# Performance work log

Hardware: AMD Instinct MI355X
Metric: run time of the kernel (lower is better)

## Reference

```python
import jax, jax.numpy as jnp
import numpy as np

D_MODEL = 1024
NUM_HEADS = 16
DEPTH = D_MODEL // NUM_HEADS


def setup_inputs() -> dict:
    key = jax.random.key(0)
    k_x, k_wqkv, k_bqkv, k_wp, k_bp = jax.random.split(key, 5)
    B, N = 2, 2048
    x = jax.random.normal(k_x, (B, N, D_MODEL), dtype=jnp.float32)
    scale = 1.0 / np.sqrt(D_MODEL)
    Wqkv = jax.random.normal(k_wqkv, (D_MODEL, 3 * D_MODEL), dtype=jnp.float32) * scale
    bqkv = jnp.zeros((3 * D_MODEL,), dtype=jnp.float32)
    Wproj = jax.random.normal(k_wp, (D_MODEL, D_MODEL), dtype=jnp.float32) * scale
    bproj = jnp.zeros((D_MODEL,), dtype=jnp.float32)
    return {"x": x, "Wqkv": Wqkv, "bqkv": bqkv, "Wproj": Wproj, "bproj": bproj}


def reference(x, Wqkv, bqkv, Wproj, bproj):
    B, N, C = x.shape
    # QKV projection; original layout: [B, N, H, depth, 3] -> transpose to [B, 3, H, N, depth]
    qkv = x @ Wqkv + bqkv                      # [B, N, 3C]
    qkv = qkv.reshape(B, N, NUM_HEADS, DEPTH, 3)
    qkv = jnp.transpose(qkv, (0, 4, 2, 1, 3))  # [B, 3, H, N, depth]
    q, k, v = qkv[:, 0], qkv[:, 1], qkv[:, 2]  # each [B, H, N, depth]
    # scaled dot-product attention (full N x N scores, as in the original)
    scale = 1.0 / jnp.sqrt(jnp.asarray(DEPTH, dtype=x.dtype))
    attn = jnp.einsum("bhnd,bhmd->bhnm", q, k) * scale
    attn = jax.nn.softmax(attn.astype(jnp.float32), axis=-1).astype(x.dtype)
    out = jnp.einsum("bhnm,bhmd->bhnd", attn, v)  # [B, H, N, depth]
    out = jnp.transpose(out, (0, 2, 1, 3)).reshape(B, N, C)
    return out @ Wproj + bproj
```

## Files before the change

kernel.cpp:

```cpp
#include <hip/hip_runtime.h>
#include <stdint.h>

#define D_MODEL 1024
#define NHEADS  16
#define DEPTH   64
#define BATCH   2
#define SEQ     2048
#define M_TOK   (BATCH*SEQ)

typedef __attribute__((ext_vector_type(8)))  short short8;
typedef __attribute__((ext_vector_type(4)))  float f32x4;
typedef __attribute__((ext_vector_type(16))) float f32x16;
typedef __attribute__((ext_vector_type(4)))  unsigned int uint4v;

#if defined(__has_builtin)
#if __has_builtin(__builtin_amdgcn_exp2f)
#define EXP2(x) __builtin_amdgcn_exp2f(x)
#endif
#endif
#ifndef EXP2
#define EXP2(x) exp2f(x)
#endif

__device__ __forceinline__ unsigned short f2bf(float f) {
  unsigned int u = __float_as_uint(f);
  u += 0x7fffu + ((u >> 16) & 1u);
  return (unsigned short)(u >> 16);
}

__device__ __forceinline__ unsigned int cvt_pk_bf16(float lo, float hi) {
  unsigned int r;
  asm("v_cvt_pk_bf16_f32 %0, %1, %2" : "=v"(r) : "v"(lo), "v"(hi));
  return r;
}

__device__ __forceinline__ void gload_lds16(const unsigned short* g, unsigned short* l) {
  __builtin_amdgcn_global_load_lds((const __attribute__((address_space(1))) void*)g,
                                   (__attribute__((address_space(3))) void*)l, 16, 0, 0);
}

__global__ void mha_prep(const float* __restrict__ x, const float* __restrict__ Wqkv,
                         const float* __restrict__ Wproj,
                         unsigned short* __restrict__ xb,
                         unsigned short* __restrict__ wqkT,
                         unsigned short* __restrict__ wvT,
                         unsigned short* __restrict__ wpT) {
  __shared__ float tile[32][33];
  int id = blockIdx.x, t = threadIdx.x;
  if (id < 2048) {
    int i = (id * 256 + t) * 8;
    float4 a = *(const float4*)(x + i);
    float4 b = *(const float4*)(x + i + 4);
    uint4 r;
    r.x = (unsigned)f2bf(a.x) | ((unsigned)f2bf(a.y) << 16);
    r.y = (unsigned)f2bf(a.z) | ((unsigned)f2bf(a.w) << 16);
    r.z = (unsigned)f2bf(b.x) | ((unsigned)f2bf(b.y) << 16);
    r.w = (unsigned)f2bf(b.z) | ((unsigned)f2bf(b.w) << 16);
    *(uint4*)(xb + i) = r;
  } else if (id < 5120) {
    int b = id - 2048;
    int c0 = (b % 96) * 32, k0 = (b / 96) * 32;
    int tx = t & 31, ty = t >> 5;
    for (int i = ty; i < 32; i += 8)
      tile[i][tx] = Wqkv[(size_t)(k0 + i) * 3072 + c0 + tx];
    __syncthreads();
    for (int i = ty; i < 32; i += 8) {
      int c = c0 + i;
      int hd = c / 3;
      int s = c - hd * 3;
      unsigned short v = f2bf(tile[tx][i]);
      if (s < 2) wqkT[(size_t)(s * 1024 + hd) * 1024 + k0 + tx] = v;
      else       wvT [(size_t)hd * 1024 + k0 + tx] = v;
    }
  } else {
    int b = id - 5120;
    int c0 = (b & 31) * 32, k0 = (b >> 5) * 32;
    int tx = t & 31, ty = t >> 5;
    for (int i = ty; i < 32; i += 8)
      tile[i][tx] = Wproj[(size_t)(k0 + i) * 1024 + c0 + tx];
    __syncthreads();
    for (int i = ty; i < 32; i += 8)
      wpT[(size_t)(c0 + i) * 1024 + k0 + tx] = f2bf(tile[tx][i]);
  }
}

__global__ __launch_bounds__(256, 3) void mha_gemm_qkv(
    const unsigned short* __restrict__ xb,
    const unsigned short* __restrict__ wqkT,
    const unsigned short* __restrict__ wvT,
    const float* __restrict__ bias,
    unsigned short* __restrict__ Qb,
    unsigned short* __restrict__ Kb,
    unsigned short* __restrict__ Vtb)
{
  __shared__ __align__(16) unsigned short As[128 * 64];
  __shared__ __align__(16) unsigned short Bs[128 * 64];
  const int K = 1024;
  int id = blockIdx.x;
  bool m0 = id < 512;
  int bx, by, bz = 0;
  const unsigned short *A, *Bt;
  if (m0) {
    int xcd = id & 7, idx = id >> 3;
    by = xcd * 4 + (idx >> 4);
    bx = idx & 15;
    A = xb; Bt = wqkT;
  } else {
    int b2 = id - 512;
    bx = b2 & 15; by = (b2 >> 4) & 7; bz = b2 >> 7;
    A = wvT; Bt = xb + (size_t)bz * SEQ * D_MODEL;
  }
  int t = threadIdx.x;
  int wv = t >> 6, lane = t & 63;
  int l15 = lane & 15, l4 = lane >> 4;
  int wr = wv >> 1, wc = wv & 1;
  int blkM = by * 128, blkN = bx * 128;

  f32x4 acc[4][4];
  for (int m = 0; m < 4; m++) for (int n = 0; n < 4; n++) acc[m][n] = (f32x4){0.f,0.f,0.f,0.f};

  for (int kt = 0; kt < K; kt += 64) {
    #pragma unroll
    for (int i = 0; i < 4; i++) {
      int e = i * 256 + t;
      int row = e >> 3;
      int sc = ((e & 7) ^ (row & 7)) * 8;
      gload_lds16(A  + (size_t)(blkM + row) * K + kt + sc, As + e * 8);
      gload_lds16(Bt + (size_t)(blkN + row) * K + kt + sc, Bs + e * 8);
    }
    __syncthreads();
    #pragma unroll
    for (int kk = 0; kk < 2; kk++) {
      int gp = ((kk * 4 + l4) ^ (l15 & 7)) * 8;
      short8 af[4], bf[4];
      #pragma unroll
      for (int m = 0; m < 4; m++)
        af[m] = *(const short8*)&As[(wr * 64 + m * 16 + l15) * 64 + gp];
      #pragma unroll
      for (int n = 0; n < 4; n++)
        bf[n] = *(const short8*)&Bs[(wc * 64 + n * 16 + l15) * 64 + gp];
      #pragma unroll
      for (int m = 0; m < 4; m++)
        #pragma unroll
        for (int n = 0; n < 4; n++)
          acc[m][n] = __builtin_amdgcn_mfma_f32_16x16x32_bf16(af[m], bf[n], acc[m][n], 0, 0, 0);
    }
    __syncthreads();
  }

  int row0 = blkM + wr * 64;
  int col0 = blkN + wc * 64;
  #pragma unroll
  for (int m = 0; m < 4; m++) {
    #pragma unroll
    for (int n = 0; n < 4; n++) {
      int colb = col0 + n * 16 + l15;
      #pragma unroll
      for (int j = 0; j < 4; j++) {
        int row = row0 + m * 16 + l4 * 4 + j;
        float v = acc[m][n][j];
        if (m0) {
          int s = colb >> 10, hd = colb & 1023;
          v += bias[hd * 3 + s];
          if (s == 0) v *= 0.18033688011112042f;
          size_t idx = ((size_t)((row >> 11) * NHEADS + (hd >> 6)) * SEQ + (row & 2047)) * DEPTH + (hd & 63);
          (s == 0 ? Qb : Kb)[idx] = f2bf(v);
        } else {
          v += bias[row * 3 + 2];
          Vtb[((size_t)(bz * 1024 + row)) * SEQ + colb] = f2bf(v);
        }
      }
    }
  }
}

__global__ __launch_bounds__(256, 3) void mha_gemm_proj(
    const unsigned short* __restrict__ A,
    const unsigned short* __restrict__ Bt,
    const float* __restrict__ bias,
    float* __restrict__ out_f)
{
  __shared__ __align__(16) unsigned short As[128 * 64];
  __shared__ __align__(16) unsigned short Bs[64 * 64];
  const int K = 1024;
  int id = blockIdx.x;
  int xcd = id & 7, idx = id >> 3;
  int by = xcd * 4 + (idx >> 4);
  int bx = idx & 15;
  int t = threadIdx.x;
  int wv = t >> 6, lane = t & 63;
  int l15 = lane & 15, l4 = lane >> 4;
  int wr = wv >> 1, wc = wv & 1;
  int blkM = by * 128, blkN = bx * 64;

  f32x4 acc[4][2];
  for (int m = 0; m < 4; m++) for (int n = 0; n < 2; n++) acc[m][n] = (f32x4){0.f,0.f,0.f,0.f};

  for (int kt = 0; kt < K; kt += 64) {
    #pragma unroll
    for (int i = 0; i < 4; i++) {
      int e = i * 256 + t;
      int row = e >> 3;
      int sc = ((e & 7) ^ (row & 7)) * 8;
      gload_lds16(A + (size_t)(blkM + row) * K + kt + sc, As + e * 8);
    }
    #pragma unroll
    for (int i = 0; i < 2; i++) {
      int e = i * 256 + t;
      int row = e >> 3;
      int sc = ((e & 7) ^ (row & 7)) * 8;
      gload_lds16(Bt + (size_t)(blkN + row) * K + kt + sc, Bs + e * 8);
    }
    __syncthreads();
    #pragma unroll
    for (int kk = 0; kk < 2; kk++) {
      int gp = ((kk * 4 + l4) ^ (l15 & 7)) * 8;
      short8 af[4], bf[2];
      #pragma unroll
      for (int m = 0; m < 4; m++)
        af[m] = *(const short8*)&As[(wr * 64 + m * 16 + l15) * 64 + gp];
      #pragma unroll
      for (int n = 0; n < 2; n++)
        bf[n] = *(const short8*)&Bs[(wc * 32 + n * 16 + l15) * 64 + gp];
      #pragma unroll
      for (int m = 0; m < 4; m++)
        #pragma unroll
        for (int n = 0; n < 2; n++)
          acc[m][n] = __builtin_amdgcn_mfma_f32_16x16x32_bf16(af[m], bf[n], acc[m][n], 0, 0, 0);
    }
    __syncthreads();
  }

  int row0 = blkM + wr * 64;
  int col0 = blkN + wc * 32;
  #pragma unroll
  for (int m = 0; m < 4; m++) {
    #pragma unroll
    for (int n = 0; n < 2; n++) {
      int colb = col0 + n * 16 + l15;
      #pragma unroll
      for (int j = 0; j < 4; j++) {
        int row = row0 + m * 16 + l4 * 4 + j;
        out_f[(size_t)row * D_MODEL + colb] = acc[m][n][j] + bias[colb];
      }
    }
  }
}

__global__ __launch_bounds__(512, 2) void mha_attn(
    const unsigned short* __restrict__ Q,
    const unsigned short* __restrict__ Kb,
    const unsigned short* __restrict__ Vt,
    unsigned short* __restrict__ O)
{
  const int N = SEQ;
  const int NIT = N / 64;
  int id = blockIdx.x;
  int bh    = (id & 7) * 4 + ((id >> 7) & 3);
  int qtile = (id >> 3) & 15;
  int t = threadIdx.x, wv = t >> 6, lane = t & 63;
  int l31 = lane & 31, hi = lane >> 5;
  int kh = wv & 1, qh = wv >> 1;

  __shared__ __align__(16) unsigned short SMEM[2 * 8192];
  __shared__ float CMB[4][64][33];

  const unsigned short* Kbh = Kb + (size_t)bh * N * DEPTH;
  const unsigned short* Vbh = Vt + (size_t)bh * DEPTH * N;

  int qrow = qtile * 128 + qh * 32 + l31;
  const unsigned short* Qp = Q + ((size_t)bh * N + qrow) * DEPTH + hi * 8;
  short8 qf[4];
  #pragma unroll
  for (int c = 0; c < 4; c++) qf[c] = *(const short8*)(Qp + c * 16);

  int srow = t >> 3;
  int sc8  = ((t & 7) ^ (srow & 7)) * 8;
  const unsigned short* kst = Kbh + (size_t)srow * DEPTH + sc8;
  const unsigned short* vst = Vbh + (size_t)srow * N + sc8;

  int rbK = (kh * 32 + l31) * 64;
  int rbV0 = l31 * 64, rbV1 = rbV0 + 2048;
  int goQK[4], goPV[2];
  #pragma unroll
  for (int c = 0; c < 4; c++) goQK[c] = ((c * 2 + hi) ^ (l31 & 7)) * 8;
  #pragma unroll
  for (int lc = 0; lc < 2; lc++) goPV[lc] = ((kh * 4 + lc * 2 + hi) ^ (l31 & 7)) * 8;

  short8 ones;
  #pragma unroll
  for (int i = 0; i < 8; i++) ones[i] = (short)0x3F80;

  f32x16 o0, o1, lsacc, zc;
  #pragma unroll
  for (int i = 0; i < 16; i++) { o0[i] = 0.f; o1[i] = 0.f; lsacc[i] = 0.f; zc[i] = 0.f; }

  gload_lds16(kst, SMEM + t * 8);
  gload_lds16(vst, SMEM + 4096 + t * 8);
  asm volatile("s_waitcnt vmcnt(0)" ::: "memory");
  __builtin_amdgcn_sched_barrier(0);
  __builtin_amdgcn_s_barrier();
  __builtin_amdgcn_sched_barrier(0);

#define BODY(BUF, IT)                                                                   \
  do {                                                                                  \
    if ((IT) + 1 < NIT) {                                                               \
      gload_lds16(kst + (size_t)((IT) + 1) * 4096, SMEM + ((BUF) ^ 1) * 8192 + t * 8);  \
      gload_lds16(vst + ((IT) + 1) * 64, SMEM + ((BUF) ^ 1) * 8192 + 4096 + t * 8);     \
    }                                                                                   \
    {                                                                                   \
      const unsigned short* Kc = SMEM + (BUF) * 8192;                                   \
      const unsigned short* Vc = Kc + 4096;                                             \
      __builtin_amdgcn_s_setprio(1);                                                    \
      short8 ka0 = *(const short8*)&Kc[rbK + goQK[0]];                                  \
      f32x16 s = __builtin_amdgcn_mfma_f32_32x32x16_bf16(ka0, qf[0], zc, 0, 0, 0);      \
      _Pragma("unroll") for (int c = 1; c < 4; c++) {                                   \
        short8 ka = *(const short8*)&Kc[rbK + goQK[c]];                                 \
        s = __builtin_amdgcn_mfma_f32_32x32x16_bf16(ka, qf[c], s, 0, 0, 0);             \
      }                                                                                 \
      __builtin_amdgcn_s_setprio(0);                                                    \
      float p[16];                                                                      \
      _Pragma("unroll") for (int r = 0; r < 16; r++) p[r] = EXP2(s[r]);                 \
      _Pragma("unroll") for (int lc = 0; lc < 2; lc++) {                                \
        unsigned int X0 = cvt_pk_bf16(p[8*lc+0], p[8*lc+1]);                            \
        unsigned int X1 = cvt_pk_bf16(p[8*lc+2], p[8*lc+3]);                            \
        unsigned int X2 = cvt_pk_bf16(p[8*lc+4], p[8*lc+5]);                            \
        unsigned int X3 = cvt_pk_bf16(p[8*lc+6], p[8*lc+7]);                            \
        auto r02 = __builtin_amdgcn_permlane32_swap(X0, X2, false, false);              \
        auto r13 = __builtin_amdgcn_permlane32_swap(X1, X3, false, false);              \
        uint4v wvec; wvec[0] = r02[0]; wvec[1] = r13[0]; wvec[2] = r02[1]; wvec[3] = r13[1]; \
        short8 bfrag = __builtin_bit_cast(short8, wvec);                                \
        short8 va = *(const short8*)&Vc[rbV0 + goPV[lc]];                               \
        short8 vb = *(const short8*)&Vc[rbV1 + goPV[lc]];                               \
        __builtin_amdgcn_s_setprio(1);                                                  \
        o0 = __builtin_amdgcn_mfma_f32_32x32x16_bf16(va, bfrag, o0, 0, 0, 0);           \
        o1 = __builtin_amdgcn_mfma_f32_32x32x16_bf16(vb, bfrag, o1, 0, 0, 0);           \
        lsacc = __builtin_amdgcn_mfma_f32_32x32x16_bf16(ones, bfrag, lsacc, 0, 0, 0);   \
        __builtin_amdgcn_s_setprio(0);                                                  \
      }                                                                                 \
    }                                                                                   \
    if ((IT) + 1 < NIT) {                                                               \
      asm volatile("s_waitcnt vmcnt(0)" ::: "memory");                                  \
      __builtin_amdgcn_sched_barrier(0);                                                \
      __builtin_amdgcn_s_barrier();                                                     \
      __builtin_amdgcn_sched_barrier(0);                                                \
    }                                                                                   \
  } while (0)

  for (int it2 = 0; it2 < NIT; it2 += 2) {
    BODY(0, it2);
    BODY(1, it2 + 1);
  }
#undef BODY

  float ls = lsacc[0];

  if (kh == 1) {
    float* c0 = &CMB[qh][lane][0];
    #pragma unroll
    for (int i = 0; i < 16; i++) { c0[i] = o0[i]; c0[16 + i] = o1[i]; }
    c0[32] = ls;
  }
  __syncthreads();
  if (kh == 0) {
    const float* c0 = &CMB[qh][lane][0];
    #pragma unroll
    for (int i = 0; i < 16; i++) { o0[i] += c0[i]; o1[i] += c0[16 + i]; }
    float rl = 1.0f / (ls + c0[32]);

    int b = bh >> 4, h = bh & 15;
    unsigned short* Op = O + ((size_t)b * N + qrow) * D_MODEL + h * DEPTH;
    #pragma unroll
    for (int gq = 0; gq < 4; gq++) {
      #pragma unroll
      for (int rp = 0; rp < 2; rp++) {
        int reg = gq * 4 + rp * 2;
        int d = gq * 8 + hi * 4 + rp * 2;
        *(unsigned int*)(Op + d)      = cvt_pk_bf16(o0[reg] * rl, o0[reg + 1] * rl);
        *(unsigned int*)(Op + 32 + d) = cvt_pk_bf16(o1[reg] * rl, o1[reg + 1] * rl);
      }
    }
  }
}

extern "C" void kernel_launch(void* const* d_in, const int* in_sizes, int n_in,
                              void* d_out, int out_size, void* d_ws, size_t ws_size,
                              hipStream_t stream) {
  const float* x     = (const float*)d_in[0];
  const float* Wqkv  = (const float*)d_in[1];
  const float* bqkv  = (const float*)d_in[2];
  const float* Wproj = (const float*)d_in[3];
  const float* bproj = (const float*)d_in[4];
  float* out = (float*)d_out;

  char* w = (char*)d_ws;
  unsigned short* xb    = (unsigned short*)(w);
  unsigned short* wqkT  = (unsigned short*)(w + 8388608);
  unsigned short* wvT   = (unsigned short*)(w + 8388608 + 4194304);
  unsigned short* wpT   = (unsigned short*)(w + 8388608 + 4194304 + 2097152);
  unsigned short* Qbuf  = (unsigned short*)(w + 16777216);
  unsigned short* Kbuf  = (unsigned short*)(w + 16777216 + 8388608);
  unsigned short* Vtb   = (unsigned short*)(w + 16777216 + 16777216);
  unsigned short* AOut  = (unsigned short*)(w + 16777216 + 25165824);

  mha_prep<<<6144, 256, 0, stream>>>(x, Wqkv, Wproj, xb, wqkT, wvT, wpT);
  mha_gemm_qkv<<<768, 256, 0, stream>>>(xb, wqkT, wvT, bqkv, Qbuf, Kbuf, Vtb);
  mha_attn<<<512, 512, 0, stream>>>(Qbuf, Kbuf, Vtb, AOut);
  mha_gemm_proj<<<512, 256, 0, stream>>>(AOut, wpT, bproj, out);
}
```

Before: 111.3 us.

## Double KV tile to 128 keys per iteration and alias combine buffer onto SMEM

The attention loop now stages 128 keys of K and V per iteration instead of 64. That halves the number of barrier and wait synchronisations and issues four async loads per stage. Each iteration runs two 64-key sub-groups of QK, exp and PV MFMAs, with the per-wave key split adjusted to match. The separate cross-wave combine array is removed; it now reuses the doubled K/V shared buffer after an added syncthreads. The change raises LDS use per block to 64KB, which may affect occupancy at two blocks per CU, and changes the V swizzle layout.

```diff
diff --git a/kernel.cpp b/kernel.cpp
--- a/kernel.cpp
+++ b/kernel.cpp
@@ -254,7 +254,7 @@
     unsigned short* __restrict__ O)
 {
   const int N = SEQ;
-  const int NIT = N / 64;
+  const int NIT = N / 128;
   int id = blockIdx.x;
   int bh    = (id & 7) * 4 + ((id >> 7) & 3);
   int qtile = (id >> 3) & 15;
@@ -262,8 +262,7 @@
   int l31 = lane & 31, hi = lane >> 5;
   int kh = wv & 1, qh = wv >> 1;
 
-  __shared__ __align__(16) unsigned short SMEM[2 * 8192];
-  __shared__ float CMB[4][64][33];
+  __shared__ __align__(16) unsigned short SMEM[2 * 16384];
 
   const unsigned short* Kbh = Kb + (size_t)bh * N * DEPTH;
   const unsigned short* Vbh = Vt + (size_t)bh * DEPTH * N;
@@ -274,18 +273,24 @@
   #pragma unroll
   for (int c = 0; c < 4; c++) qf[c] = *(const short8*)(Qp + c * 16);
 
-  int srow = t >> 3;
-  int sc8  = ((t & 7) ^ (srow & 7)) * 8;
-  const unsigned short* kst = Kbh + (size_t)srow * DEPTH + sc8;
-  const unsigned short* vst = Vbh + (size_t)srow * N + sc8;
-
-  int rbK = (kh * 32 + l31) * 64;
-  int rbV0 = l31 * 64, rbV1 = rbV0 + 2048;
-  int goQK[4], goPV[2];
+  int krow = t >> 3;
+  int ksc  = ((t & 7) ^ (krow & 7)) * 8;
+  const unsigned short* kst = Kbh + (size_t)krow * DEPTH + ksc;
+  int vrow = t >> 4;
+  int vg   = t & 15;
+  int vsc  = ((vg ^ (vrow & 7))) * 8;
+  const unsigned short* vst = Vbh + (size_t)vrow * N + vsc;
+
+  int rbK0 = (kh * 64 + l31) * 64;
+  int rbV0 = l31 * 128, rbV1 = rbV0 + 4096;
+  int goQK[4], goPV[4];
   #pragma unroll
   for (int c = 0; c < 4; c++) goQK[c] = ((c * 2 + hi) ^ (l31 & 7)) * 8;
   #pragma unroll
-  for (int lc = 0; lc < 2; lc++) goPV[lc] = ((kh * 4 + lc * 2 + hi) ^ (l31 & 7)) * 8;
+  for (int i = 0; i < 4; i++) {
+    int g = i >> 1, lc = i & 1;
+    goPV[i] = ((kh * 8 + g * 4 + lc * 2 + hi) ^ (l31 & 7)) * 8;
+  }
 
   short8 ones;
   #pragma unroll
@@ -295,56 +300,65 @@
   #pragma unroll
   for (int i = 0; i < 16; i++) { o0[i] = 0.f; o1[i] = 0.f; lsacc[i] = 0.f; zc[i] = 0.f; }
 
-  gload_lds16(kst, SMEM + t * 8);
-  gload_lds16(vst, SMEM + 4096 + t * 8);
+  gload_lds16(kst,                       SMEM + t * 8);
+  gload_lds16(kst + 4096,                SMEM + 4096 + t * 8);
+  gload_lds16(vst,                       SMEM + 8192 + t * 8);
+  gload_lds16(vst + (size_t)32 * N,      SMEM + 12288 + t * 8);
   asm volatile("s_waitcnt vmcnt(0)" ::: "memory");
   __builtin_amdgcn_sched_barrier(0);
   __builtin_amdgcn_s_barrier();
   __builtin_amdgcn_sched_barrier(0);
 
-#define BODY(BUF, IT)                                                                   \
-  do {                                                                                  \
-    if ((IT) + 1 < NIT) {                                                               \
-      gload_lds16(kst + (size_t)((IT) + 1) * 4096, SMEM + ((BUF) ^ 1) * 8192 + t * 8);  \
-      gload_lds16(vst + ((IT) + 1) * 64, SMEM + ((BUF) ^ 1) * 8192 + 4096 + t * 8);     \
-    }                                                                                   \
-    {                                                                                   \
-      const unsigned short* Kc = SMEM + (BUF) * 8192;                                   \
-      const unsigned short* Vc = Kc + 4096;                                             \
-      __builtin_amdgcn_s_setprio(1);                                                    \
-      short8 ka0 = *(const short8*)&Kc[rbK + goQK[0]];                                  \
-      f32x16 s = __builtin_amdgcn_mfma_f32_32x32x16_bf16(ka0, qf[0], zc, 0, 0, 0);      \
-      _Pragma("unroll") for (int c = 1; c < 4; c++) {                                   \
-        short8 ka = *(const short8*)&Kc[rbK + goQK[c]];                                 \
-        s = __builtin_amdgcn_mfma_f32_32x32x16_bf16(ka, qf[c], s, 0, 0, 0);             \
-      }                                                                                 \
-      __builtin_amdgcn_s_setprio(0);                                                    \
-      float p[16];                                                                      \
-      _Pragma("unroll") for (int r = 0; r < 16; r++) p[r] = EXP2(s[r]);                 \
-      _Pragma("unroll") for (int lc = 0; lc < 2; lc++) {                                \
-        unsigned int X0 = cvt_pk_bf16(p[8*lc+0], p[8*lc+1]);                            \
-        unsigned int X1 = cvt_pk_bf16(p[8*lc+2], p[8*lc+3]);                            \
-        unsigned int X2 = cvt_pk_bf16(p[8*lc+4], p[8*lc+5]);                            \
-        unsigned int X3 = cvt_pk_bf16(p[8*lc+6], p[8*lc+7]);                            \
-        auto r02 = __builtin_amdgcn_permlane32_swap(X0, X2, false, false);              \
-        auto r13 = __builtin_amdgcn_permlane32_swap(X1, X3, false, false);              \
-        uint4v wvec; wvec[0] = r02[0]; wvec[1] = r13[0]; wvec[2] = r02[1]; wvec[3] = r13[1]; \
-        short8 bfrag = __builtin_bit_cast(short8, wvec);                                \
-        short8 va = *(const short8*)&Vc[rbV0 + goPV[lc]];                               \
-        short8 vb = *(const short8*)&Vc[rbV1 + goPV[lc]];                               \
-        __builtin_amdgcn_s_setprio(1);                                                  \
-        o0 = __builtin_amdgcn_mfma_f32_32x32x16_bf16(va, bfrag, o0, 0, 0, 0);           \
-        o1 = __builtin_amdgcn_mfma_f32_32x32x16_bf16(vb, bfrag, o1, 0, 0, 0);           \
-        lsacc = __builtin_amdgcn_mfma_f32_32x32x16_bf16(ones, bfrag, lsacc, 0, 0, 0);   \
-        __builtin_amdgcn_s_setprio(0);                                                  \
-      }                                                                                 \
-    }                                                                                   \
-    if ((IT) + 1 < NIT) {                                                               \
-      asm volatile("s_waitcnt vmcnt(0)" ::: "memory");                                  \
-      __builtin_amdgcn_sched_barrier(0);                                                \
-      __builtin_amdgcn_s_barrier();                                                     \
-      __builtin_amdgcn_sched_barrier(0);                                                \
-    }                                                                                   \
+#define BODY(BUF, IT)                                                                     \
+  do {                                                                                    \
+    if ((IT) + 1 < NIT) {                                                                 \
+      unsigned short* nb = SMEM + ((BUF) ^ 1) * 16384;                                    \
+      const unsigned short* kn = kst + (size_t)((IT) + 1) * 8192;                         \
+      const unsigned short* vn = vst + ((IT) + 1) * 128;                                  \
+      gload_lds16(kn,                  nb + t * 8);                                       \
+      gload_lds16(kn + 4096,           nb + 4096 + t * 8);                                \
+      gload_lds16(vn,                  nb + 8192 + t * 8);                                \
+      gload_lds16(vn + (size_t)32 * N, nb + 12288 + t * 8);                               \
+    }                                                                                     \
+    {                                                                                     \
+      const unsigned short* Kc = SMEM + (BUF) * 16384;                                    \
+      const unsigned short* Vc = Kc + 8192;                                               \
+      _Pragma("unroll") for (int g = 0; g < 2; g++) {                                     \
+        __builtin_amdgcn_s_setprio(1);                                                    \
+        short8 ka0 = *(const short8*)&Kc[rbK0 + g * 2048 + goQK[0]];                      \
+        f32x16 s = __builtin_amdgcn_mfma_f32_32x32x16_bf16(ka0, qf[0], zc, 0, 0, 0);      \
+        _Pragma("unroll") for (int c = 1; c < 4; c++) {                                   \
+          short8 ka = *(const short8*)&Kc[rbK0 + g * 2048 + goQK[c]];                     \
+          s = __builtin_amdgcn_mfma_f32_32x32x16_bf16(ka, qf[c], s, 0, 0, 0);             \
+        }                                                                                 \
+        __builtin_amdgcn_s_setprio(0);                                                    \
+        float p[16];                                                                      \
+        _Pragma("unroll") for (int r = 0; r < 16; r++) p[r] = EXP2(s[r]);                 \
+        _Pragma("unroll") for (int lc = 0; lc < 2; lc++) {                                \
+          unsigned int X0 = cvt_pk_bf16(p[8*lc+0], p[8*lc+1]);                            \
+          unsigned int X1 = cvt_pk_bf16(p[8*lc+2], p[8*lc+3]);                            \
+          unsigned int X2 = cvt_pk_bf16(p[8*lc+4], p[8*lc+5]);                            \
+          unsigned int X3 = cvt_pk_bf16(p[8*lc+6], p[8*lc+7]);                            \
+          auto r02 = __builtin_amdgcn_permlane32_swap(X0, X2, false, false);              \
+          auto r13 = __builtin_amdgcn_permlane32_swap(X1, X3, false, false);              \
+          uint4v wvec; wvec[0] = r02[0]; wvec[1] = r13[0]; wvec[2] = r02[1]; wvec[3] = r13[1]; \
+          short8 bfrag = __builtin_bit_cast(short8, wvec);                                \
+          short8 va = *(const short8*)&Vc[rbV0 + goPV[g * 2 + lc]];                       \
+          short8 vb = *(const short8*)&Vc[rbV1 + goPV[g * 2 + lc]];                       \
+          __builtin_amdgcn_s_setprio(1);                                                  \
+          o0 = __builtin_amdgcn_mfma_f32_32x32x16_bf16(va, bfrag, o0, 0, 0, 0);           \
+          o1 = __builtin_amdgcn_mfma_f32_32x32x16_bf16(vb, bfrag, o1, 0, 0, 0);           \
+          lsacc = __builtin_amdgcn_mfma_f32_32x32x16_bf16(ones, bfrag, lsacc, 0, 0, 0);   \
+          __builtin_amdgcn_s_setprio(0);                                                  \
+        }                                                                                 \
+      }                                                                                   \
+    }                                                                                     \
+    if ((IT) + 1 < NIT) {                                                                 \
+      asm volatile("s_waitcnt vmcnt(0)" ::: "memory");                                    \
+      __builtin_amdgcn_sched_barrier(0);                                                  \
+      __builtin_amdgcn_s_barrier();                                                       \
+      __builtin_amdgcn_sched_barrier(0);                                                  \
+    }                                                                                     \
   } while (0)
 
   for (int it2 = 0; it2 < NIT; it2 += 2) {
@@ -355,15 +369,17 @@
 
   float ls = lsacc[0];
 
+  __syncthreads();
+  float* cmb = (float*)SMEM;
   if (kh == 1) {
-    float* c0 = &CMB[qh][lane][0];
+    float* c0 = cmb + (qh * 64 + lane) * 33;
     #pragma unroll
     for (int i = 0; i < 16; i++) { c0[i] = o0[i]; c0[16 + i] = o1[i]; }
     c0[32] = ls;
   }
   __syncthreads();
   if (kh == 0) {
-    const float* c0 = &CMB[qh][lane][0];
+    const float* c0 = cmb + (qh * 64 + lane) * 33;
     #pragma unroll
     for (int i = 0; i < 16; i++) { o0[i] += c0[i]; o1[i] += c0[16 + i]; }
     float rl = 1.0f / (ls + c0[32]);
```

After: 110.8 us, median of 2. Within noise of the previous version (-0.5%).

## Triple-buffer K/V tiles in LDS and alias combine buffer onto staging memory

Applied to the files above, without the earlier changes.

Switches the attention K/V staging from double to triple buffering with a prefetch distance of two tiles, using partial vmcnt waits so the next tile's loads can remain in flight across the barrier. The cross-wave combine buffer now reuses the staging LDS after an extra sync instead of a separate allocation, keeping total LDS lower. The goal is to hide global load latency better; the cost is more LDS per block, runtime buffer index rotation instead of a compile-time unrolled pair, and an additional barrier.

```diff
diff --git a/kernel.cpp b/kernel.cpp
--- a/kernel.cpp
+++ b/kernel.cpp
@@ -262,8 +262,7 @@
   int l31 = lane & 31, hi = lane >> 5;
   int kh = wv & 1, qh = wv >> 1;
 
-  __shared__ __align__(16) unsigned short SMEM[2 * 8192];
-  __shared__ float CMB[4][64][33];
+  __shared__ __align__(16) unsigned short SMEM[3 * 8192];
 
   const unsigned short* Kbh = Kb + (size_t)bh * N * DEPTH;
   const unsigned short* Vbh = Vt + (size_t)bh * DEPTH * N;
@@ -295,75 +294,82 @@
   #pragma unroll
   for (int i = 0; i < 16; i++) { o0[i] = 0.f; o1[i] = 0.f; lsacc[i] = 0.f; zc[i] = 0.f; }
 
-  gload_lds16(kst, SMEM + t * 8);
-  gload_lds16(vst, SMEM + 4096 + t * 8);
-  asm volatile("s_waitcnt vmcnt(0)" ::: "memory");
+#define STAGE(buf, kt)                                                                  \
+  do {                                                                                  \
+    unsigned short* base = SMEM + (buf) * 8192;                                         \
+    gload_lds16(kst + (size_t)(kt) * DEPTH, base + t * 8);                              \
+    gload_lds16(vst + (kt),                 base + 4096 + t * 8);                       \
+  } while (0)
+
+  STAGE(0, 0);
+  STAGE(1, 64);
+  asm volatile("s_waitcnt vmcnt(2)" ::: "memory");
   __builtin_amdgcn_sched_barrier(0);
   __builtin_amdgcn_s_barrier();
   __builtin_amdgcn_sched_barrier(0);
 
-#define BODY(BUF, IT)                                                                   \
-  do {                                                                                  \
-    if ((IT) + 1 < NIT) {                                                               \
-      gload_lds16(kst + (size_t)((IT) + 1) * 4096, SMEM + ((BUF) ^ 1) * 8192 + t * 8);  \
-      gload_lds16(vst + ((IT) + 1) * 64, SMEM + ((BUF) ^ 1) * 8192 + 4096 + t * 8);     \
-    }                                                                                   \
-    {                                                                                   \
-      const unsigned short* Kc = SMEM + (BUF) * 8192;                                   \
-      const unsigned short* Vc = Kc + 4096;                                             \
-      __builtin_amdgcn_s_setprio(1);                                                    \
-      short8 ka0 = *(const short8*)&Kc[rbK + goQK[0]];                                  \
-      f32x16 s = __builtin_amdgcn_mfma_f32_32x32x16_bf16(ka0, qf[0], zc, 0, 0, 0);      \
-      _Pragma("unroll") for (int c = 1; c < 4; c++) {                                   \
-        short8 ka = *(const short8*)&Kc[rbK + goQK[c]];                                 \
-        s = __builtin_amdgcn_mfma_f32_32x32x16_bf16(ka, qf[c], s, 0, 0, 0);             \
-      }                                                                                 \
-      __builtin_amdgcn_s_setprio(0);                                                    \
-      float p[16];                                                                      \
-      _Pragma("unroll") for (int r = 0; r < 16; r++) p[r] = EXP2(s[r]);                 \
-      _Pragma("unroll") for (int lc = 0; lc < 2; lc++) {                                \
-        unsigned int X0 = cvt_pk_bf16(p[8*lc+0], p[8*lc+1]);                            \
-        unsigned int X1 = cvt_pk_bf16(p[8*lc+2], p[8*lc+3]);                            \
-        unsigned int X2 = cvt_pk_bf16(p[8*lc+4], p[8*lc+5]);                            \
-        unsigned int X3 = cvt_pk_bf16(p[8*lc+6], p[8*lc+7]);                            \
-        auto r02 = __builtin_amdgcn_permlane32_swap(X0, X2, false, false);              \
-        auto r13 = __builtin_amdgcn_permlane32_swap(X1, X3, false, false);              \
-        uint4v wvec; wvec[0] = r02[0]; wvec[1] = r13[0]; wvec[2] = r02[1]; wvec[3] = r13[1]; \
-        short8 bfrag = __builtin_bit_cast(short8, wvec);                                \
-        short8 va = *(const short8*)&Vc[rbV0 + goPV[lc]];                               \
-        short8 vb = *(const short8*)&Vc[rbV1 + goPV[lc]];                               \
-        __builtin_amdgcn_s_setprio(1);                                                  \
-        o0 = __builtin_amdgcn_mfma_f32_32x32x16_bf16(va, bfrag, o0, 0, 0, 0);           \
-        o1 = __builtin_amdgcn_mfma_f32_32x32x16_bf16(vb, bfrag, o1, 0, 0, 0);           \
-        lsacc = __builtin_amdgcn_mfma_f32_32x32x16_bf16(ones, bfrag, lsacc, 0, 0, 0);   \
-        __builtin_amdgcn_s_setprio(0);                                                  \
-      }                                                                                 \
-    }                                                                                   \
-    if ((IT) + 1 < NIT) {                                                               \
-      asm volatile("s_waitcnt vmcnt(0)" ::: "memory");                                  \
-      __builtin_amdgcn_sched_barrier(0);                                                \
-      __builtin_amdgcn_s_barrier();                                                     \
-      __builtin_amdgcn_sched_barrier(0);                                                \
-    }                                                                                   \
-  } while (0)
-
-  for (int it2 = 0; it2 < NIT; it2 += 2) {
-    BODY(0, it2);
-    BODY(1, it2 + 1);
-  }
-#undef BODY
+  int cur = 0, sb = 2;
+  for (int it = 0; it < NIT; ++it) {
+    if (it + 2 < NIT) STAGE(sb, (it + 2) * 64);
+    {
+      const unsigned short* Kc = SMEM + cur * 8192;
+      const unsigned short* Vc = Kc + 4096;
+      __builtin_amdgcn_s_setprio(1);
+      short8 ka0 = *(const short8*)&Kc[rbK + goQK[0]];
+      f32x16 s = __builtin_amdgcn_mfma_f32_32x32x16_bf16(ka0, qf[0], zc, 0, 0, 0);
+      #pragma unroll
+      for (int c = 1; c < 4; c++) {
+        short8 ka = *(const short8*)&Kc[rbK + goQK[c]];
+        s = __builtin_amdgcn_mfma_f32_32x32x16_bf16(ka, qf[c], s, 0, 0, 0);
+      }
+      __builtin_amdgcn_s_setprio(0);
+      float p[16];
+      #pragma unroll
+      for (int r = 0; r < 16; r++) p[r] = EXP2(s[r]);
+      #pragma unroll
+      for (int lc = 0; lc < 2; lc++) {
+        unsigned int X0 = cvt_pk_bf16(p[8*lc+0], p[8*lc+1]);
+        unsigned int X1 = cvt_pk_bf16(p[8*lc+2], p[8*lc+3]);
+        unsigned int X2 = cvt_pk_bf16(p[8*lc+4], p[8*lc+5]);
+        unsigned int X3 = cvt_pk_bf16(p[8*lc+6], p[8*lc+7]);
+        auto r02 = __builtin_amdgcn_permlane32_swap(X0, X2, false, false);
+        auto r13 = __builtin_amdgcn_permlane32_swap(X1, X3, false, false);
+        uint4v wvec; wvec[0] = r02[0]; wvec[1] = r13[0]; wvec[2] = r02[1]; wvec[3] = r13[1];
+        short8 bfrag = __builtin_bit_cast(short8, wvec);
+        short8 va = *(const short8*)&Vc[rbV0 + goPV[lc]];
+        short8 vb = *(const short8*)&Vc[rbV1 + goPV[lc]];
+        __builtin_amdgcn_s_setprio(1);
+        o0 = __builtin_amdgcn_mfma_f32_32x32x16_bf16(va, bfrag, o0, 0, 0, 0);
+        o1 = __builtin_amdgcn_mfma_f32_32x32x16_bf16(vb, bfrag, o1, 0, 0, 0);
+        lsacc = __builtin_amdgcn_mfma_f32_32x32x16_bf16(ones, bfrag, lsacc, 0, 0, 0);
+        __builtin_amdgcn_s_setprio(0);
+      }
+    }
+    if (it < NIT - 1) {
+      if (it + 2 < NIT) asm volatile("s_waitcnt vmcnt(2)" ::: "memory");
+      else              asm volatile("s_waitcnt vmcnt(0)" ::: "memory");
+      __builtin_amdgcn_sched_barrier(0);
+      __builtin_amdgcn_s_barrier();
+      __builtin_amdgcn_sched_barrier(0);
+    }
+    cur = (cur == 2) ? 0 : cur + 1;
+    sb  = (sb  == 2) ? 0 : sb  + 1;
+  }
+#undef STAGE
 
   float ls = lsacc[0];
 
+  __syncthreads();
+  float* cmb = (float*)SMEM;
   if (kh == 1) {
-    float* c0 = &CMB[qh][lane][0];
+    float* c0 = cmb + (qh * 64 + lane) * 33;
     #pragma unroll
     for (int i = 0; i < 16; i++) { c0[i] = o0[i]; c0[16 + i] = o1[i]; }
     c0[32] = ls;
   }
   __syncthreads();
   if (kh == 0) {
-    const float* c0 = &CMB[qh][lane][0];
+    const float* c0 = cmb + (qh * 64 + lane) * 33;
     #pragma unroll
     for (int i = 0; i < 16; i++) { o0[i] += c0[i]; o1[i] += c0[16 + i]; }
     float rl = 1.0f / (ls + c0[32]);
```

After: 111.0 us. About the same (-0.3%).
